# Kernel tuning notes

Hardware: AMD Instinct MI355X
Metric: run time of the kernel (lower is better)

Reference implementation:

```python
import jax, jax.numpy as jnp
import numpy as np

C1, C2, NHEAD = 256, 512, 8
HEAD_DIM = C1 // NHEAD
LN_EPS = 1e-5
L2_EPS = 1e-4
RMS_EPS = 1e-6
BN_EPS = 1e-5


def _linear(x, w, b):
    return x @ w.T + b


def _layernorm(x, w, b):
    mu = jnp.mean(x, axis=-1, keepdims=True)
    var = jnp.mean((x - mu) ** 2, axis=-1, keepdims=True)
    return (x - mu) / jnp.sqrt(var + LN_EPS) * w + b


def _rmsnorm(x, w):
    rms = jnp.sqrt(jnp.mean(x * x, axis=-1, keepdims=True) + RMS_EPS)
    return w * x / rms


def _l2norm(x):
    n = jnp.sqrt(jnp.sum(x * x, axis=-1, keepdims=True))
    return x / jnp.maximum(n, L2_EPS)


def _avg_pool(x, k):
    b, c, h, w = x.shape
    return x.reshape(b, c, h // k, k, w // k, k).mean(axis=(3, 5))


def _pos_embed_2d(w_, h_, dim, temperature=10000.0):
    # mirrors build_2d_sincos_position_embedding(w, h, embed_dim) called as (h, w, c)
    pos_dim = dim // 4
    omega = 1.0 / temperature ** (jnp.arange(pos_dim, dtype=jnp.float32) / pos_dim)
    gw, gh = jnp.meshgrid(jnp.arange(w_, dtype=jnp.float32),
                          jnp.arange(h_, dtype=jnp.float32), indexing='ij')
    ow = gw.reshape(-1, 1) * omega[None, :]
    oh = gh.reshape(-1, 1) * omega[None, :]
    return jnp.concatenate([jnp.sin(ow), jnp.cos(ow), jnp.sin(oh), jnp.cos(oh)], axis=1)  # [h*w, dim]


def setup_inputs() -> dict:
    key = jax.random.key(0)
    ks = jax.random.split(key, 32)
    p = lambda i, shape, s=0.02: jax.random.normal(ks[i], shape, dtype=jnp.float32) * s
    return {
        'a3': jax.random.normal(ks[0], (8, C1, 112, 112), dtype=jnp.float32),
        'a4': jax.random.normal(ks[1], (8, C2, 56, 56), dtype=jnp.float32),
        'conv_w': p(2, (C1, C2)), 'conv_b': p(3, (C1,)),
        'bn_w': 1.0 + p(4, (C1,)), 'bn_b': p(5, (C1,)),
        'q_w': p(6, (C1, C1)), 'q_b': p(7, (C1,)),
        'q_ln_w': 1.0 + p(8, (C1,)), 'q_ln_b': p(9, (C1,)),
        'k_w': p(10, (C1, C1)), 'k_b': p(11, (C1,)),
        'k_ln_w': 1.0 + p(12, (C1,)), 'k_ln_b': p(13, (C1,)),
        'v_w': p(14, (C1, C1)), 'v_b': p(15, (C1,)),
        'o_w': p(16, (C1, C1)), 'o_b': p(17, (C1,)),
        'rms_w': 1.0 + p(18, (HEAD_DIM,)),
        'l1_w': p(19, (4 * C1, C1)), 'l1_b': p(20, (4 * C1,)),
        'l2_w': p(21, (C1, 4 * C1)), 'l2_b': p(22, (C1,)),
        'n1_w': 1.0 + p(23, (C1,)), 'n1_b': p(24, (C1,)),
        'n2_w': 1.0 + p(25, (C1,)), 'n2_b': p(26, (C1,)),
        'idx': 10,
    }


def reference(a3, a4, conv_w, conv_b, bn_w, bn_b, q_w, q_b, q_ln_w, q_ln_b,
              k_w, k_b, k_ln_w, k_ln_b, v_w, v_b, o_w, o_b, rms_w,
              l1_w, l1_b, l2_w, l2_b, n1_w, n1_b, n2_w, n2_b, idx):
    # high_to_low_embed: 1x1 conv + BatchNorm2d (eval mode, running mean/var = 0/1)
    a4e = jnp.einsum('bchw,oc->bohw', a4, conv_w) + conv_b[None, :, None, None]
    a4e = a4e / np.float32(np.sqrt(1.0 + BN_EPS)) * bn_w[None, :, None, None] + bn_b[None, :, None, None]
    if idx == 10:
        a3_down = _avg_pool(a3, 2)
    else:
        a3_down = _avg_pool(a3, 4)
        a4e = _avg_pool(a4e, 2)
    b, c, h, w = a3_down.shape
    L = h * w
    residual = a3_down.reshape(b, c, L).transpose(0, 2, 1)   # [b, L, c]
    a3f = a3_down.reshape(b, c, L).transpose(2, 0, 1)        # [L, b, c]
    a4f = a4e.reshape(b, c, -1).transpose(2, 0, 1)           # [L, b, c]
    pos = _pos_embed_2d(h, w, c)[:, None, :]                 # [L, 1, c]
    a3f = a3f + pos
    a4f = a4f + pos
    Q = _layernorm(_linear(a3f, q_w, q_b), q_ln_w, q_ln_b)
    K = _layernorm(_linear(a4f, k_w, k_b), k_ln_w, k_ln_b)
    V = _linear(a4f, v_w, v_b)
    Q = _l2norm(Q)
    K = _l2norm(K)
    Q = Q.reshape(L, b * NHEAD, HEAD_DIM).transpose(1, 0, 2)  # [b*h, L, d]
    K = K.reshape(L, b * NHEAD, HEAD_DIM).transpose(1, 0, 2)
    V = V.reshape(L, b * NHEAD, HEAD_DIM).transpose(1, 0, 2)
    # cosFormer-style sin/cos positional reweighting (src_len == tgt_len here)
    wi = (jnp.arange(1, L + 1, dtype=jnp.float32) / L)[None, :, None]
    sw, cw = jnp.sin(wi), jnp.cos(wi)
    Q_ = jnp.concatenate([Q * cw, Q * sw], axis=-1)          # [b*h, L, 2d]
    K_ = jnp.concatenate([K * cw, K * sw], axis=-1)
    KV = jnp.einsum('nld,nlm->ndm', K_, V)                   # [b*h, 2d, d]
    attn = jnp.einsum('nld,ndm->nlm', Q_, KV)                # [b*h, L, d]
    attn = _rmsnorm(attn, rms_w)
    attn = attn.reshape(b, NHEAD, L, HEAD_DIM).transpose(2, 0, 1, 3).reshape(L, b, c)
    out = _linear(attn, o_w, o_b).transpose(1, 0, 2)         # [b, L, c]
    out = residual + _layernorm(out, n1_w, n1_b)
    residual2 = out
    ffn = _linear(jax.nn.gelu(_linear(out, l1_w, l1_b), approximate=False), l2_w, l2_b)
    out = residual2 + _layernorm(ffn, n2_w, n2_b)
    a3_sa = out.transpose(0, 2, 1).reshape(b, c, h, w)
    a3_sa = jax.image.resize(a3_sa, a3.shape, method='bilinear')  # align_corners=False
    a3_sa = a3_sa * a3
    b4, c4, h4, w4 = a4.shape
    a4_up = jax.image.resize(a4, (b4, c4, 2 * h4, 2 * w4), method='bilinear')
    return (a3_sa, a4_up)
```

## Files before the change

### kernel.cpp

```cpp
#include <hip/hip_runtime.h>
#include <math.h>

#define L_    3136
#define R_    25088
#define C_    256
#define MATF  6422528

typedef __attribute__((ext_vector_type(8))) short s16x8;
typedef __attribute__((ext_vector_type(4))) float f32x4;
typedef unsigned short us;

__device__ __forceinline__ us bfh(float v) {
    unsigned u = __float_as_uint(v);
    u = (u + 0x7FFFu + ((u >> 16) & 1u)) >> 16;
    return (us)u;
}
__device__ __forceinline__ float bf2f(us h) { return __uint_as_float((unsigned)h << 16); }
__device__ __forceinline__ void split2(float v, us& h, us& l) {
    h = bfh(v);
    l = bfh(v - bf2f(h));
}
__device__ __forceinline__ uint4 packu4(const us* s) {
    uint4 u;
    u.x = (unsigned)s[0] | ((unsigned)s[1] << 16);
    u.y = (unsigned)s[2] | ((unsigned)s[3] << 16);
    u.z = (unsigned)s[4] | ((unsigned)s[5] << 16);
    u.w = (unsigned)s[6] | ((unsigned)s[7] << 16);
    return u;
}
__device__ __forceinline__ uint2 packu2(const us* s) {
    uint2 u;
    u.x = (unsigned)s[0] | ((unsigned)s[1] << 16);
    u.y = (unsigned)s[2] | ((unsigned)s[3] << 16);
    return u;
}

__device__ __forceinline__ void gl16(const us* g, const us* l) {
    __builtin_amdgcn_global_load_lds(
        (const __attribute__((address_space(1))) unsigned int*)(unsigned long long)(const void*)g,
        (__attribute__((address_space(3))) unsigned int*)(unsigned int)(unsigned long long)(const void*)l,
        16, 0, 0);
}

__device__ __forceinline__ void wconv_body(const float* __restrict__ src,
        us* __restrict__ dh, us* __restrict__ dl, int idx, int kgs, int K)
{
    int m  = idx >> kgs;
    int gk = idx & ((1 << kgs) - 1);
    const float* sp = src + (size_t)m * K + gk * 8;
    float4 v0 = *(const float4*)sp;
    float4 v1 = *(const float4*)(sp + 4);
    float vv[8] = {v0.x, v0.y, v0.z, v0.w, v1.x, v1.y, v1.z, v1.w};
    us hh[8], ll[8];
    #pragma unroll
    for (int e = 0; e < 8; e++) split2(vv[e], hh[e], ll[e]);
    int p = gk ^ ((m >> 1) & 7);
    size_t off = (size_t)m * K + (size_t)p * 8;
    *(uint4*)(dh + off) = packu4(hh);
    *(uint4*)(dl + off) = packu4(ll);
}

__global__ __launch_bounds__(256)
void wconv1_k(const float* __restrict__ w, us* __restrict__ dh, us* __restrict__ dl)
{
    wconv_body(w, dh, dl, blockIdx.x * 256 + threadIdx.x, 6, 512);
}

__global__ __launch_bounds__(256)
void wconv6_k(const float* __restrict__ q, const float* __restrict__ k,
              const float* __restrict__ v, const float* __restrict__ o,
              const float* __restrict__ l1, const float* __restrict__ l2,
              us* __restrict__ wb)
{
    int bid = blockIdx.x;
    const float* src; us* dh; us* dl; int kgs, K;
    if (bid < 32)       { src = q;  dh = wb;           dl = wb + 65536;   kgs = 5; K = 256;  }
    else if (bid < 64)  { src = k;  dh = wb + 131072;  dl = wb + 196608;  kgs = 5; K = 256;  bid -= 32;  }
    else if (bid < 96)  { src = v;  dh = wb + 262144;  dl = wb + 327680;  kgs = 5; K = 256;  bid -= 64;  }
    else if (bid < 128) { src = o;  dh = wb + 393216;  dl = wb + 458752;  kgs = 5; K = 256;  bid -= 96;  }
    else if (bid < 256) { src = l1; dh = wb + 524288;  dl = wb + 786432;  kgs = 5; K = 256;  bid -= 128; }
    else                { src = l2; dh = wb + 1048576; dl = wb + 1310720; kgs = 7; K = 1024; bid -= 256; }
    wconv_body(src, dh, dl, bid * 256 + threadIdx.x, kgs, K);
}

__global__ __launch_bounds__(256)
void tconv_k(const float* __restrict__ src, us* __restrict__ dh, us* __restrict__ dl,
             int C, int Lb)
{
    __shared__ float tl[64][68];
    int l0 = blockIdx.x * 64, c0 = blockIdx.y * 64, b = blockIdx.z;
    int t = threadIdx.x;
    {
        int cl = t >> 2, qq = t & 3;
        const float* sp = src + ((size_t)b * C + c0 + cl) * Lb + l0 + qq * 16;
        #pragma unroll
        for (int i = 0; i < 4; i++) {
            float4 v = *(const float4*)(sp + i * 4);
            *(float4*)&tl[cl][qq * 16 + i * 4] = v;
        }
    }
    __syncthreads();
    int rl = t & 63, cq = t >> 6;
    size_t r = (size_t)b * Lb + l0 + rl;
    int s3 = ((l0 + rl) >> 1) & 7;
    size_t rowo = r * (size_t)C;
    #pragma unroll
    for (int half = 0; half < 2; half++) {
        us hh[8], ll[8];
        #pragma unroll
        for (int e = 0; e < 8; e++)
            split2(tl[cq * 16 + half * 8 + e][rl], hh[e], ll[e]);
        int gfull = (c0 >> 3) + cq * 2 + half;
        int p = gfull ^ s3;
        *(uint4*)(dh + rowo + (size_t)p * 8) = packu4(hh);
        *(uint4*)(dl + rowo + (size_t)p * 8) = packu4(ll);
    }
}

#define GBM 128
#define GBN 64
#define GBK 64
enum { GE_F32 = 0, GE_CONVT = 1, GE_GELUT = 2 };

template<int EPI>
__global__ __launch_bounds__(256)
void gemm_mf(const us* __restrict__ Wh, const us* __restrict__ Wl,
             const us* __restrict__ Xh, const us* __restrict__ Xl,
             float* __restrict__ Yf, us* __restrict__ Yth, us* __restrict__ Ytl,
             const float* __restrict__ bias, const float* __restrict__ bnw,
             const float* __restrict__ bnb, const float* __restrict__ pos,
             int K, int mts, int Mrow)
{
    __shared__ us Ah[GBM * GBK];
    __shared__ us Al[GBM * GBK];
    __shared__ us Bh[GBN * GBK];
    __shared__ us Bl[GBN * GBK];

    const int tid = threadIdx.x;
    int nwg = gridDim.x;
    int wg = (blockIdx.x & 7) * (nwg >> 3) + (blockIdx.x >> 3);
    int mt = wg & ((1 << mts) - 1);
    int rt = wg >> mts;
    const int m0 = mt * GBM;
    const int r0 = rt * GBN;

    const us* Ahg = Wh + (size_t)m0 * K;
    const us* Alg = Wl + (size_t)m0 * K;
    const us* Bhg = Xh + (size_t)r0 * K;
    const us* Blg = Xl + (size_t)r0 * K;

    const int lane = tid & 63;
    const int w    = tid >> 6;
    const int wm   = (w >> 1) * 64;
    const int wr   = (w & 1) * 32;
    const int l15  = lane & 15;
    const int lg   = lane >> 4;

    f32x4 acc[4][2];
    #pragma unroll
    for (int a = 0; a < 4; a++)
        #pragma unroll
        for (int b = 0; b < 2; b++)
            acc[a][b] = (f32x4){0.f, 0.f, 0.f, 0.f};

    for (int k0 = 0; k0 < K; k0 += GBK) {
        #pragma unroll
        for (int q = 0; q < 4; q++) {
            int g = q * 256 + tid;
            int row = g >> 3, sub = (g & 7) << 3;
            gl16(Ahg + (size_t)row * K + k0 + sub, Ah + g * 8);
            gl16(Alg + (size_t)row * K + k0 + sub, Al + g * 8);
        }
        #pragma unroll
        for (int q = 0; q < 2; q++) {
            int g = q * 256 + tid;
            int row = g >> 3, sub = (g & 7) << 3;
            gl16(Bhg + (size_t)row * K + k0 + sub, Bh + g * 8);
            gl16(Blg + (size_t)row * K + k0 + sub, Bl + g * 8);
        }
        __syncthreads();
        #pragma unroll
        for (int kk = 0; kk < 2; kk++) {
            s16x8 ah[4], al[4], bh[2], bl[2];
            #pragma unroll
            for (int a = 0; a < 4; a++) {
                int row = wm + a * 16 + l15;
                int p = ((kk << 2) | lg) ^ ((row >> 1) & 7);
                ah[a] = *(const s16x8*)(Ah + row * GBK + p * 8);
                al[a] = *(const s16x8*)(Al + row * GBK + p * 8);
            }
            #pragma unroll
            for (int b = 0; b < 2; b++) {
                int row = wr + b * 16 + l15;
                int p = ((kk << 2) | lg) ^ ((row >> 1) & 7);
                bh[b] = *(const s16x8*)(Bh + row * GBK + p * 8);
                bl[b] = *(const s16x8*)(Bl + row * GBK + p * 8);
            }
            #pragma unroll
            for (int a = 0; a < 4; a++)
                #pragma unroll
                for (int b = 0; b < 2; b++) {
                    acc[a][b] = __builtin_amdgcn_mfma_f32_16x16x32_bf16(ah[a], bh[b], acc[a][b], 0, 0, 0);
                    acc[a][b] = __builtin_amdgcn_mfma_f32_16x16x32_bf16(ah[a], bl[b], acc[a][b], 0, 0, 0);
                    acc[a][b] = __builtin_amdgcn_mfma_f32_16x16x32_bf16(al[a], bh[b], acc[a][b], 0, 0, 0);
                }
        }
        __syncthreads();
    }

    if (EPI == GE_F32) {
        #pragma unroll
        for (int a = 0; a < 4; a++) {
            int mb = m0 + wm + a * 16 + lg * 4;
            #pragma unroll
            for (int b = 0; b < 2; b++) {
                int rr = r0 + wr + b * 16 + l15;
                #pragma unroll
                for (int q = 0; q < 4; q++)
                    Yf[(size_t)(mb + q) * R_ + rr] = acc[a][b][q] + bias[mb + q];
            }
        }
    } else {
        #pragma unroll
        for (int b = 0; b < 2; b++) {
            int rr = r0 + wr + b * 16 + l15;
            int s3 = (rr >> 1) & 7;
            int l = rr % L_;
            size_t rowo = (size_t)rr * Mrow;
            #pragma unroll
            for (int a = 0; a < 4; a++) {
                int mb = m0 + wm + a * 16 + lg * 4;
                us hh[4], ll[4];
                #pragma unroll
                for (int q = 0; q < 4; q++) {
                    int m = mb + q;
                    float v = acc[a][b][q] + bias[m];
                    if (EPI == GE_CONVT) {
                        v = v * 0.9999950000374997f * bnw[m] + bnb[m];
                        v += pos[(size_t)m * L_ + l];
                    } else {
                        v = 0.5f * v * (1.f + erff(v * 0.7071067811865475f));
                    }
                    split2(v, hh[q], ll[q]);
                }
                int p = (mb >> 3) ^ s3;
                size_t off = rowo + (size_t)((p << 3) | (mb & 7));
                *(uint2*)(Yth + off) = packu2(hh);
                *(uint2*)(Ytl + off) = packu2(ll);
            }
        }
    }
}

__global__ __launch_bounds__(256)
void pos_k(float* __restrict__ pos)
{
    int c = blockIdx.x;
    int q = c >> 6, t = c & 63;
    float om = exp2f(-(float)t * (13.287712379549449f / 64.f));
    for (int l = threadIdx.x; l < L_; l += 256) {
        int y = l / 56, x = l - y * 56;
        float arg = (q < 2 ? (float)y : (float)x) * om;
        pos[(size_t)c * L_ + l] = (q & 1) ? cosf(arg) : sinf(arg);
    }
}

__global__ __launch_bounds__(256)
void pool_k(const float* __restrict__ a3, const float* __restrict__ pos,
            float* __restrict__ a3d, us* __restrict__ xh, us* __restrict__ xl)
{
    __shared__ us hi[256][34];
    __shared__ us lo[256][34];
    int blk = blockIdx.x;
    int b = blk / 98, l0 = (blk % 98) * 32;
    int t = threadIdx.x;
    {
        int lt = t & 31, cg = t >> 5;
        int l = l0 + lt;
        int y = l / 56, x = l - y * 56;
        const float* srow = a3 + ((size_t)b * 256) * 12544 + (2 * y) * 112 + 2 * x;
        float* drow = a3d + (size_t)b * L_ + l;
        const float* prow = pos + l;
        for (int cc = 0; cc < 32; cc++) {
            int c = cc * 8 + cg;
            const float* sp = srow + (size_t)c * 12544;
            float2 v0 = *(const float2*)sp;
            float2 v1 = *(const float2*)(sp + 112);
            float v = (v0.x + v0.y + v1.x + v1.y) * 0.25f;
            drow[(size_t)c * R_] = v;
            split2(v + prow[(size_t)c * L_], hi[c][lt], lo[c][lt]);
        }
    }
    __syncthreads();
    int j = t & 31, cq = t >> 5;
    int r = b * L_ + l0 + j;
    int s3 = ((l0 + j) >> 1) & 7;
    size_t rowo = (size_t)r * 256;
    #pragma unroll
    for (int gg = 0; gg < 4; gg++) {
        int cb = cq * 32 + gg * 8;
        us hh[8], ll[8];
        #pragma unroll
        for (int e = 0; e < 8; e++) { hh[e] = hi[cb + e][j]; ll[e] = lo[cb + e][j]; }
        int p = ((cq << 2) | gg) ^ s3;
        *(uint4*)(xh + rowo + (size_t)p * 8) = packu4(hh);
        *(uint4*)(xl + rowo + (size_t)p * 8) = packu4(ll);
    }
}

__global__ __launch_bounds__(256)
void ln_l2_k(float* __restrict__ X, const float* __restrict__ wt, const float* __restrict__ bt)
{
    __shared__ float red[4][64];
    __shared__ float red2[4][64];
    int tid = threadIdx.x;
    int rr = tid & 63, og = tid >> 6;
    size_t r = (size_t)blockIdx.x * 64 + rr;
    float s1 = 0.f, s2 = 0.f;
    for (int j = 0; j < 64; j++) {
        float v = X[(size_t)(og * 64 + j) * R_ + r];
        s1 += v; s2 = fmaf(v, v, s2);
    }
    red[og][rr] = s1; red2[og][rr] = s2;
    __syncthreads();
    float mu  = (red[0][rr] + red[1][rr] + red[2][rr] + red[3][rr]) * (1.f / 256.f);
    float var = (red2[0][rr] + red2[1][rr] + red2[2][rr] + red2[3][rr]) * (1.f / 256.f) - mu * mu;
    float rstd = rsqrtf(var + 1e-5f);
    __syncthreads();
    float t2 = 0.f;
    for (int j = 0; j < 64; j++) {
        int o = og * 64 + j;
        float v = X[(size_t)o * R_ + r];
        float y = (v - mu) * rstd * wt[o] + bt[o];
        t2 = fmaf(y, y, t2);
    }
    red[og][rr] = t2;
    __syncthreads();
    float nrm = sqrtf(red[0][rr] + red[1][rr] + red[2][rr] + red[3][rr]);
    float scale = 1.f / fmaxf(nrm, 1e-4f);
    for (int j = 0; j < 64; j++) {
        int o = og * 64 + j;
        size_t ix = (size_t)o * R_ + r;
        float v = X[ix];
        X[ix] = (v - mu) * rstd * wt[o] * scale + bt[o] * scale;
    }
}

template<int TOUT>
__global__ __launch_bounds__(256)
void ln_res_k(float* __restrict__ X, const float* __restrict__ res,
              const float* __restrict__ wt, const float* __restrict__ bt,
              us* __restrict__ th, us* __restrict__ tl_)
{
    __shared__ float red[4][64];
    __shared__ float red2[4][64];
    int tid = threadIdx.x;
    int rr = tid & 63, og = tid >> 6;
    size_t r = (size_t)blockIdx.x * 64 + rr;
    float s1 = 0.f, s2 = 0.f;
    for (int j = 0; j < 64; j++) {
        float v = X[(size_t)(og * 64 + j) * R_ + r];
        s1 += v; s2 = fmaf(v, v, s2);
    }
    red[og][rr] = s1; red2[og][rr] = s2;
    __syncthreads();
    float mu  = (red[0][rr] + red[1][rr] + red[2][rr] + red[3][rr]) * (1.f / 256.f);
    float var = (red2[0][rr] + red2[1][rr] + red2[2][rr] + red2[3][rr]) * (1.f / 256.f) - mu * mu;
    float rstd = rsqrtf(var + 1e-5f);
    float yv[64];
    #pragma unroll
    for (int j = 0; j < 64; j++) {
        int o = og * 64 + j;
        size_t ix = (size_t)o * R_ + r;
        float v = X[ix];
        float y = res[ix] + (v - mu) * rstd * wt[o] + bt[o];
        X[ix] = y;
        yv[j] = y;
    }
    if (TOUT) {
        int s3 = ((int)r >> 1) & 7;
        size_t rowo = r * 256;
        #pragma unroll
        for (int g = 0; g < 8; g++) {
            us hh[8], ll[8];
            #pragma unroll
            for (int e = 0; e < 8; e++) split2(yv[g * 8 + e], hh[e], ll[e]);
            int p = ((og << 3) | g) ^ s3;
            *(uint4*)(th  + rowo + (size_t)p * 8) = packu4(hh);
            *(uint4*)(tl_ + rowo + (size_t)p * 8) = packu4(ll);
        }
    }
}

__global__ __launch_bounds__(256)
void kv_part_k(const float* __restrict__ Kt, const float* __restrict__ Vt,
               float* __restrict__ kvp)
{
    __shared__ float kl[64][33];
    __shared__ float vl[64][33];
    __shared__ float cwl[64], swl[64];
    int slab = blockIdx.x;
    int n = blockIdx.y;
    int b = n >> 3, h = n & 7;
    int tid = threadIdx.x;
    int lane = tid & 63, grp = tid >> 6;
    int d = tid >> 2;
    int m0 = (tid & 3) * 8;
    float acc[8] = {0,0,0,0,0,0,0,0};
    size_t base = (size_t)(h * 32) * R_ + (size_t)b * L_;
    for (int ch = 0; ch < 7; ch++) {
        int l0 = slab * 448 + ch * 64;
        #pragma unroll
        for (int j = 0; j < 8; j++) {
            int dd = grp * 8 + j;
            kl[lane][dd] = Kt[base + (size_t)dd * R_ + l0 + lane];
            vl[lane][dd] = Vt[base + (size_t)dd * R_ + l0 + lane];
        }
        if (tid < 64) {
            float wi = (float)(l0 + tid + 1) * (1.f / 3136.f);
            cwl[tid] = cosf(wi); swl[tid] = sinf(wi);
        }
        __syncthreads();
        for (int l = 0; l < 64; l++) {
            float kvv = (d < 32 ? cwl[l] : swl[l]) * kl[l][d & 31];
            #pragma unroll
            for (int j = 0; j < 8; j++)
                acc[j] = fmaf(kvv, vl[l][m0 + j], acc[j]);
        }
        __syncthreads();
    }
    float* out = kvp + ((size_t)(n * 7 + slab)) * 2048 + d * 32 + m0;
    #pragma unroll
    for (int j = 0; j < 8; j++) out[j] = acc[j];
}

__global__ __launch_bounds__(256)
void kv_red_k(const float* __restrict__ kvp, float* __restrict__ kv)
{
    int idx = blockIdx.x * 256 + threadIdx.x;
    int n = idx >> 11, dm = idx & 2047;
    float s = 0.f;
    #pragma unroll
    for (int t = 0; t < 7; t++) s += kvp[((size_t)(n * 7 + t)) * 2048 + dm];
    kv[idx] = s;
}

__global__ __launch_bounds__(256)
void attn_k(const float* __restrict__ Q, const float* __restrict__ kv,
            const float* __restrict__ rmsw, us* __restrict__ Gh, us* __restrict__ Gl)
{
    __shared__ float kvl[2048];
    int h = blockIdx.y, b = blockIdx.z;
    int tid = threadIdx.x;
    int n = b * 8 + h;
    for (int i = tid; i < 2048; i += 256) kvl[i] = kv[(size_t)n * 2048 + i];
    __syncthreads();
    int l = blockIdx.x * 256 + tid;
    if (l >= L_) return;
    size_t r = (size_t)b * L_ + l;
    float qd[32];
    #pragma unroll
    for (int dd = 0; dd < 32; dd++) qd[dd] = Q[((size_t)(h * 32 + dd)) * R_ + r];
    float wi = (float)(l + 1) * (1.f / 3136.f);
    float cw = cosf(wi), sw = sinf(wi);
    float val[32]; float ss = 0.f;
    #pragma unroll
    for (int m = 0; m < 32; m++) {
        float s1 = 0.f, s2 = 0.f;
        #pragma unroll
        for (int dd = 0; dd < 32; dd++) {
            s1 = fmaf(qd[dd], kvl[dd * 32 + m], s1);
            s2 = fmaf(qd[dd], kvl[(dd + 32) * 32 + m], s2);
        }
        float v = cw * s1 + sw * s2;
        val[m] = v; ss = fmaf(v, v, ss);
    }
    float rinv = rsqrtf(ss * (1.f / 32.f) + 1e-6f);
    int s3 = (l >> 1) & 7;
    size_t rowo = r * 256;
    #pragma unroll
    for (int j = 0; j < 4; j++) {
        us hh[8], ll[8];
        #pragma unroll
        for (int e = 0; e < 8; e++) {
            float y = rmsw[j * 8 + e] * val[j * 8 + e] * rinv;
            split2(y, hh[e], ll[e]);
        }
        int p = ((h << 2) | j) ^ s3;
        *(uint4*)(Gh + rowo + (size_t)p * 8) = packu4(hh);
        *(uint4*)(Gl + rowo + (size_t)p * 8) = packu4(ll);
    }
}

__device__ __forceinline__ void bil_coord(int o, int lim, int& i0, int& i1, float& t)
{
    float f = o * 0.5f - 0.25f;
    float fl = floorf(f);
    t = f - fl;
    int i = (int)fl;
    i0 = i < 0 ? 0 : (i > lim ? lim : i);
    int ip = i + 1;
    i1 = ip < 0 ? 0 : (ip > lim ? lim : ip);
}

__global__ __launch_bounds__(256)
void up_a3_k(const float* __restrict__ out2, const float* __restrict__ a3,
             float* __restrict__ out)
{
    unsigned idx = blockIdx.x * 256u + threadIdx.x;
    int xo = idx % 112;
    unsigned t1 = idx / 112;
    int yo = t1 % 112;
    unsigned t2 = t1 / 112;
    int c = t2 & 255;
    int b = t2 >> 8;
    int x0, x1, y0, y1; float tx, ty;
    bil_coord(xo, 55, x0, x1, tx);
    bil_coord(yo, 55, y0, y1, ty);
    const float* src = out2 + (size_t)c * R_ + (size_t)b * L_;
    float v00 = src[y0 * 56 + x0], v01 = src[y0 * 56 + x1];
    float v10 = src[y1 * 56 + x0], v11 = src[y1 * 56 + x1];
    float v = (1.f - ty) * ((1.f - tx) * v00 + tx * v01) + ty * ((1.f - tx) * v10 + tx * v11);
    out[idx] = v * a3[idx];
}

__global__ __launch_bounds__(256)
void up_a4_k(const float* __restrict__ a4, float* __restrict__ out)
{
    unsigned idx = blockIdx.x * 256u + threadIdx.x;
    int xo = idx % 112;
    unsigned t1 = idx / 112;
    int yo = t1 % 112;
    unsigned t2 = t1 / 112;
    int c = t2 & 511;
    int b = t2 >> 9;
    int x0, x1, y0, y1; float tx, ty;
    bil_coord(xo, 55, x0, x1, tx);
    bil_coord(yo, 55, y0, y1, ty);
    const float* src = a4 + (size_t)(b * 512 + c) * 3136;
    float v00 = src[y0 * 56 + x0], v01 = src[y0 * 56 + x1];
    float v10 = src[y1 * 56 + x0], v11 = src[y1 * 56 + x1];
    out[idx] = (1.f - ty) * ((1.f - tx) * v00 + tx * v01) + ty * ((1.f - tx) * v10 + tx * v11);
}

extern "C" void kernel_launch(void* const* d_in, const int* in_sizes, int n_in,
                              void* d_out, int out_size, void* d_ws, size_t ws_size,
                              hipStream_t stream)
{
    const float* a3     = (const float*)d_in[0];
    const float* a4     = (const float*)d_in[1];
    const float* conv_w = (const float*)d_in[2];
    const float* conv_b = (const float*)d_in[3];
    const float* bn_w   = (const float*)d_in[4];
    const float* bn_b   = (const float*)d_in[5];
    const float* q_w    = (const float*)d_in[6];
    const float* q_b    = (const float*)d_in[7];
    const float* q_ln_w = (const float*)d_in[8];
    const float* q_ln_b = (const float*)d_in[9];
    const float* k_w    = (const float*)d_in[10];
    const float* k_b    = (const float*)d_in[11];
    const float* k_ln_w = (const float*)d_in[12];
    const float* k_ln_b = (const float*)d_in[13];
    const float* v_w    = (const float*)d_in[14];
    const float* v_b    = (const float*)d_in[15];
    const float* o_w    = (const float*)d_in[16];
    const float* o_b    = (const float*)d_in[17];
    const float* rms_w  = (const float*)d_in[18];
    const float* l1_w   = (const float*)d_in[19];
    const float* l1_b   = (const float*)d_in[20];
    const float* l2_w   = (const float*)d_in[21];
    const float* l2_b   = (const float*)d_in[22];
    const float* n1_w   = (const float*)d_in[23];
    const float* n1_b   = (const float*)d_in[24];
    const float* n2_w   = (const float*)d_in[25];
    const float* n2_b   = (const float*)d_in[26];
    (void)in_sizes; (void)n_in; (void)out_size;

    float* ws  = (float*)d_ws;
    float* pos = ws;
    float* P0  = ws + 802816;
    float* P1  = P0 + MATF;
    float* P2  = P1 + MATF;
    float* P3  = P2 + MATF;
    float* P4  = P3 + MATF;
    float* P5  = P4 + MATF;
    float* P6  = P5 + MATF;
    float* P7  = P6 + MATF;
    float* kvp = P7 + MATF;
    float* kvb = kvp + 917504;
    if (ws_size < (size_t)53231616 * 4) return;

    us* xqt_h = (us*)P4;  us* xqt_l = xqt_h + MATF;
    us* a4t_h = (us*)P5;  us* a4t_l = (us*)P6;
    us* Cxt_h = (us*)P1;  us* Cxt_l = Cxt_h + MATF;
    us* Gat_h = (us*)P4;  us* Gat_l = Gat_h + MATF;
    us* Hot_h = (us*)P1;  us* Hot_l = Hot_h + MATF;
    us* ffn_h = (us*)P4;  us* ffn_l = (us*)P6;
    float* Dq = P5;
    float* Ek = P6;
    float* Fv = P3;
    float* Ho = P2;
    us* wb   = (us*)pos;
    us* wc_h = (us*)kvp;  us* wc_l = wc_h + 131072;

    pos_k  <<<256, 256, 0, stream>>>(pos);
    wconv1_k<<<64, 256, 0, stream>>>(conv_w, wc_h, wc_l);
    tconv_k<<<dim3(49, 8, 8), 256, 0, stream>>>(a4, a4t_h, a4t_l, 512, 3136);
    pool_k <<<784, 256, 0, stream>>>(a3, pos, P0, xqt_h, xqt_l);
    gemm_mf<GE_CONVT><<<784, 256, 0, stream>>>(wc_h, wc_l, a4t_h, a4t_l,
        nullptr, Cxt_h, Cxt_l, conv_b, bn_w, bn_b, pos, 512, 1, 256);
    wconv6_k<<<384, 256, 0, stream>>>(q_w, k_w, v_w, o_w, l1_w, l2_w, wb);
    gemm_mf<GE_F32><<<784, 256, 0, stream>>>(wb, wb + 65536, xqt_h, xqt_l,
        Dq, nullptr, nullptr, q_b, nullptr, nullptr, nullptr, 256, 1, 256);
    ln_l2_k<<<392, 256, 0, stream>>>(Dq, q_ln_w, q_ln_b);
    gemm_mf<GE_F32><<<784, 256, 0, stream>>>(wb + 131072, wb + 196608, Cxt_h, Cxt_l,
        Ek, nullptr, nullptr, k_b, nullptr, nullptr, nullptr, 256, 1, 256);
    ln_l2_k<<<392, 256, 0, stream>>>(Ek, k_ln_w, k_ln_b);
    gemm_mf<GE_F32><<<784, 256, 0, stream>>>(wb + 262144, wb + 327680, Cxt_h, Cxt_l,
        Fv, nullptr, nullptr, v_b, nullptr, nullptr, nullptr, 256, 1, 256);
    kv_part_k<<<dim3(7, 64), 256, 0, stream>>>(Ek, Fv, kvp);
    kv_red_k<<<512, 256, 0, stream>>>(kvp, kvb);
    attn_k<<<dim3(13, 8, 8), 256, 0, stream>>>(Dq, kvb, rms_w, Gat_h, Gat_l);
    gemm_mf<GE_F32><<<784, 256, 0, stream>>>(wb + 393216, wb + 458752, Gat_h, Gat_l,
        Ho, nullptr, nullptr, o_b, nullptr, nullptr, nullptr, 256, 1, 256);
    ln_res_k<1><<<392, 256, 0, stream>>>(Ho, P0, n1_w, n1_b, Hot_h, Hot_l);
    gemm_mf<GE_GELUT><<<3136, 256, 0, stream>>>(wb + 524288, wb + 786432, Hot_h, Hot_l,
        nullptr, ffn_h, ffn_l, l1_b, nullptr, nullptr, nullptr, 256, 3, 1024);
    gemm_mf<GE_F32><<<784, 256, 0, stream>>>(wb + 1048576, wb + 1310720, ffn_h, ffn_l,
        Fv, nullptr, nullptr, l2_b, nullptr, nullptr, nullptr, 1024, 1, 256);
    ln_res_k<0><<<392, 256, 0, stream>>>(Fv, Ho, n2_w, n2_b, nullptr, nullptr);
    up_a3_k<<<100352, 256, 0, stream>>>(Fv, a3, (float*)d_out);
    up_a4_k<<<200704, 256, 0, stream>>>(a4, (float*)d_out + 25690112);
}
```

Before: 1.183 ms.

## Double-buffer GEMM LDS with BK=32, restructure upsample kernels, cache LN rows

The MFMA GEMM now uses a double-buffered LDS pipeline with a K-tile of 32, issuing the next stage's async global-to-LDS loads while the current tile is computed. The XOR swizzle is shrunk to 2 bits across every producer kernel to match the narrower tile. The two 2x bilinear upsample kernels now give each thread a 2x2 output quad with fixed 0.25/0.75 weights and vector float2 stores, so neighbouring source values are reused. ln_l2_k keeps the row in registers instead of re-reading X three times, at the cost of much higher register pressure.

```diff
diff --git a/kernel.cpp b/kernel.cpp
--- a/kernel.cpp
+++ b/kernel.cpp
@@ -42,6 +42,10 @@
         16, 0, 0);
 }
 
+__device__ __forceinline__ int swz2(int g, int s2) {
+    return (g & ~3) | ((g ^ s2) & 3);
+}
+
 __device__ __forceinline__ void wconv_body(const float* __restrict__ src,
         us* __restrict__ dh, us* __restrict__ dl, int idx, int kgs, int K)
 {
@@ -54,7 +58,7 @@
     us hh[8], ll[8];
     #pragma unroll
     for (int e = 0; e < 8; e++) split2(vv[e], hh[e], ll[e]);
-    int p = gk ^ ((m >> 1) & 7);
+    int p = swz2(gk, (m >> 1) & 3);
     size_t off = (size_t)m * K + (size_t)p * 8;
     *(uint4*)(dh + off) = packu4(hh);
     *(uint4*)(dl + off) = packu4(ll);
@@ -102,7 +106,7 @@
     __syncthreads();
     int rl = t & 63, cq = t >> 6;
     size_t r = (size_t)b * Lb + l0 + rl;
-    int s3 = ((l0 + rl) >> 1) & 7;
+    int s2 = ((l0 + rl) >> 1) & 3;
     size_t rowo = r * (size_t)C;
     #pragma unroll
     for (int half = 0; half < 2; half++) {
@@ -111,7 +115,7 @@
         for (int e = 0; e < 8; e++)
             split2(tl[cq * 16 + half * 8 + e][rl], hh[e], ll[e]);
         int gfull = (c0 >> 3) + cq * 2 + half;
-        int p = gfull ^ s3;
+        int p = swz2(gfull, s2);
         *(uint4*)(dh + rowo + (size_t)p * 8) = packu4(hh);
         *(uint4*)(dl + rowo + (size_t)p * 8) = packu4(ll);
     }
@@ -119,7 +123,7 @@
 
 #define GBM 128
 #define GBN 64
-#define GBK 64
+#define GBK 32
 enum { GE_F32 = 0, GE_CONVT = 1, GE_GELUT = 2 };
 
 template<int EPI>
@@ -131,10 +135,10 @@
              const float* __restrict__ bnb, const float* __restrict__ pos,
              int K, int mts, int Mrow)
 {
-    __shared__ us Ah[GBM * GBK];
-    __shared__ us Al[GBM * GBK];
-    __shared__ us Bh[GBN * GBK];
-    __shared__ us Bl[GBN * GBK];
+    __shared__ us Ah[2][GBM * GBK];
+    __shared__ us Al[2][GBM * GBK];
+    __shared__ us Bh[2][GBN * GBK];
+    __shared__ us Bl[2][GBN * GBK];
 
     const int tid = threadIdx.x;
     int nwg = gridDim.x;
@@ -155,6 +159,11 @@
     const int wr   = (w & 1) * 32;
     const int l15  = lane & 15;
     const int lg   = lane >> 4;
+    const int s2k  = (l15 >> 1) & 3;
+    const int koff = ((lg ^ s2k) & 3) << 3;
+
+    const int asub = (tid & 3) << 3;
+    const int brow = tid >> 2, bsub = (tid & 3) << 3;
 
     f32x4 acc[4][2];
     #pragma unroll
@@ -163,50 +172,55 @@
         for (int b = 0; b < 2; b++)
             acc[a][b] = (f32x4){0.f, 0.f, 0.f, 0.f};
 
-    for (int k0 = 0; k0 < K; k0 += GBK) {
-        #pragma unroll
-        for (int q = 0; q < 4; q++) {
-            int g = q * 256 + tid;
-            int row = g >> 3, sub = (g & 7) << 3;
-            gl16(Ahg + (size_t)row * K + k0 + sub, Ah + g * 8);
-            gl16(Alg + (size_t)row * K + k0 + sub, Al + g * 8);
-        }
-        #pragma unroll
-        for (int q = 0; q < 2; q++) {
-            int g = q * 256 + tid;
-            int row = g >> 3, sub = (g & 7) << 3;
-            gl16(Bhg + (size_t)row * K + k0 + sub, Bh + g * 8);
-            gl16(Blg + (size_t)row * K + k0 + sub, Bl + g * 8);
-        }
-        __syncthreads();
-        #pragma unroll
-        for (int kk = 0; kk < 2; kk++) {
-            s16x8 ah[4], al[4], bh[2], bl[2];
-            #pragma unroll
-            for (int a = 0; a < 4; a++) {
-                int row = wm + a * 16 + l15;
-                int p = ((kk << 2) | lg) ^ ((row >> 1) & 7);
-                ah[a] = *(const s16x8*)(Ah + row * GBK + p * 8);
-                al[a] = *(const s16x8*)(Al + row * GBK + p * 8);
-            }
+    const int nst = K >> 5;
+
+    #define STAGE(buf, k0)                                                        \
+    {                                                                             \
+        _Pragma("unroll")                                                         \
+        for (int q = 0; q < 2; q++) {                                             \
+            int g = q * 256 + tid;                                                \
+            int row = g >> 2;                                                     \
+            gl16(Ahg + (size_t)row * K + (k0) + asub, &Ah[buf][g * 8]);           \
+            gl16(Alg + (size_t)row * K + (k0) + asub, &Al[buf][g * 8]);           \
+        }                                                                         \
+        gl16(Bhg + (size_t)brow * K + (k0) + bsub, &Bh[buf][tid * 8]);            \
+        gl16(Blg + (size_t)brow * K + (k0) + bsub, &Bl[buf][tid * 8]);            \
+    }
+
+    STAGE(0, 0);
+    __syncthreads();
+    int cur = 0;
+    for (int s = 0; s < nst; s++) {
+        if (s + 1 < nst) STAGE(cur ^ 1, (s + 1) << 5);
+        const us* AHc = &Ah[cur][0];
+        const us* ALc = &Al[cur][0];
+        const us* BHc = &Bh[cur][0];
+        const us* BLc = &Bl[cur][0];
+        s16x8 va[4], wa[4], vb[2], ub[2];
+        #pragma unroll
+        for (int a = 0; a < 4; a++) {
+            int off = (wm + a * 16 + l15) * GBK + koff;
+            va[a] = *(const s16x8*)(AHc + off);
+            wa[a] = *(const s16x8*)(ALc + off);
+        }
+        #pragma unroll
+        for (int b = 0; b < 2; b++) {
+            int off = (wr + b * 16 + l15) * GBK + koff;
+            vb[b] = *(const s16x8*)(BHc + off);
+            ub[b] = *(const s16x8*)(BLc + off);
+        }
+        #pragma unroll
+        for (int a = 0; a < 4; a++)
             #pragma unroll
             for (int b = 0; b < 2; b++) {
-                int row = wr + b * 16 + l15;
-                int p = ((kk << 2) | lg) ^ ((row >> 1) & 7);
-                bh[b] = *(const s16x8*)(Bh + row * GBK + p * 8);
-                bl[b] = *(const s16x8*)(Bl + row * GBK + p * 8);
+                acc[a][b] = __builtin_amdgcn_mfma_f32_16x16x32_bf16(va[a], vb[b], acc[a][b], 0, 0, 0);
+                acc[a][b] = __builtin_amdgcn_mfma_f32_16x16x32_bf16(va[a], ub[b], acc[a][b], 0, 0, 0);
+                acc[a][b] = __builtin_amdgcn_mfma_f32_16x16x32_bf16(wa[a], vb[b], acc[a][b], 0, 0, 0);
             }
-            #pragma unroll
-            for (int a = 0; a < 4; a++)
-                #pragma unroll
-                for (int b = 0; b < 2; b++) {
-                    acc[a][b] = __builtin_amdgcn_mfma_f32_16x16x32_bf16(ah[a], bh[b], acc[a][b], 0, 0, 0);
-                    acc[a][b] = __builtin_amdgcn_mfma_f32_16x16x32_bf16(ah[a], bl[b], acc[a][b], 0, 0, 0);
-                    acc[a][b] = __builtin_amdgcn_mfma_f32_16x16x32_bf16(al[a], bh[b], acc[a][b], 0, 0, 0);
-                }
-        }
         __syncthreads();
-    }
+        cur ^= 1;
+    }
+    #undef STAGE
 
     if (EPI == GE_F32) {
         #pragma unroll
@@ -224,7 +238,7 @@
         #pragma unroll
         for (int b = 0; b < 2; b++) {
             int rr = r0 + wr + b * 16 + l15;
-            int s3 = (rr >> 1) & 7;
+            int s2r = (rr >> 1) & 3;
             int l = rr % L_;
             size_t rowo = (size_t)rr * Mrow;
             #pragma unroll
@@ -243,7 +257,7 @@
                     }
                     split2(v, hh[q], ll[q]);
                 }
-                int p = (mb >> 3) ^ s3;
+                int p = swz2(mb >> 3, s2r);
                 size_t off = rowo + (size_t)((p << 3) | (mb & 7));
                 *(uint2*)(Yth + off) = packu2(hh);
                 *(uint2*)(Ytl + off) = packu2(ll);
@@ -294,7 +308,7 @@
     __syncthreads();
     int j = t & 31, cq = t >> 5;
     int r = b * L_ + l0 + j;
-    int s3 = ((l0 + j) >> 1) & 7;
+    int s2 = ((l0 + j) >> 1) & 3;
     size_t rowo = (size_t)r * 256;
     #pragma unroll
     for (int gg = 0; gg < 4; gg++) {
@@ -302,7 +316,7 @@
         us hh[8], ll[8];
         #pragma unroll
         for (int e = 0; e < 8; e++) { hh[e] = hi[cb + e][j]; ll[e] = lo[cb + e][j]; }
-        int p = ((cq << 2) | gg) ^ s3;
+        int p = swz2((cq << 2) | gg, s2);
         *(uint4*)(xh + rowo + (size_t)p * 8) = packu4(hh);
         *(uint4*)(xl + rowo + (size_t)p * 8) = packu4(ll);
     }
@@ -310,6 +324,47 @@
 
 __global__ __launch_bounds__(256)
 void ln_l2_k(float* __restrict__ X, const float* __restrict__ wt, const float* __restrict__ bt)
+{
+    __shared__ float red[4][64];
+    __shared__ float red2[4][64];
+    int tid = threadIdx.x;
+    int rr = tid & 63, og = tid >> 6;
+    size_t r = (size_t)blockIdx.x * 64 + rr;
+    float vv[64];
+    float s1 = 0.f, s2 = 0.f;
+    for (int j = 0; j < 64; j++) {
+        float v = X[(size_t)(og * 64 + j) * R_ + r];
+        vv[j] = v;
+        s1 += v; s2 = fmaf(v, v, s2);
+    }
+    red[og][rr] = s1; red2[og][rr] = s2;
+    __syncthreads();
+    float mu  = (red[0][rr] + red[1][rr] + red[2][rr] + red[3][rr]) * (1.f / 256.f);
+    float var = (red2[0][rr] + red2[1][rr] + red2[2][rr] + red2[3][rr]) * (1.f / 256.f) - mu * mu;
+    float rstd = rsqrtf(var + 1e-5f);
+    __syncthreads();
+    float t2 = 0.f;
+    for (int j = 0; j < 64; j++) {
+        int o = og * 64 + j;
+        float y = (vv[j] - mu) * rstd * wt[o] + bt[o];
+        t2 = fmaf(y, y, t2);
+    }
+    red[og][rr] = t2;
+    __syncthreads();
+    float nrm = sqrtf(red[0][rr] + red[1][rr] + red[2][rr] + red[3][rr]);
+    float scale = 1.f / fmaxf(nrm, 1e-4f);
+    for (int j = 0; j < 64; j++) {
+        int o = og * 64 + j;
+        size_t ix = (size_t)o * R_ + r;
+        X[ix] = (vv[j] - mu) * rstd * wt[o] * scale + bt[o] * scale;
+    }
+}
+
+template<int TOUT>
+__global__ __launch_bounds__(256)
+void ln_res_k(float* __restrict__ X, const float* __restrict__ res,
+              const float* __restrict__ wt, const float* __restrict__ bt,
+              us* __restrict__ th, us* __restrict__ tl_)
 {
     __shared__ float red[4][64];
     __shared__ float red2[4][64];
@@ -326,47 +381,6 @@
     float mu  = (red[0][rr] + red[1][rr] + red[2][rr] + red[3][rr]) * (1.f / 256.f);
     float var = (red2[0][rr] + red2[1][rr] + red2[2][rr] + red2[3][rr]) * (1.f / 256.f) - mu * mu;
     float rstd = rsqrtf(var + 1e-5f);
-    __syncthreads();
-    float t2 = 0.f;
-    for (int j = 0; j < 64; j++) {
-        int o = og * 64 + j;
-        float v = X[(size_t)o * R_ + r];
-        float y = (v - mu) * rstd * wt[o] + bt[o];
-        t2 = fmaf(y, y, t2);
-    }
-    red[og][rr] = t2;
-    __syncthreads();
-    float nrm = sqrtf(red[0][rr] + red[1][rr] + red[2][rr] + red[3][rr]);
-    float scale = 1.f / fmaxf(nrm, 1e-4f);
-    for (int j = 0; j < 64; j++) {
-        int o = og * 64 + j;
-        size_t ix = (size_t)o * R_ + r;
-        float v = X[ix];
-        X[ix] = (v - mu) * rstd * wt[o] * scale + bt[o] * scale;
-    }
-}
-
-template<int TOUT>
-__global__ __launch_bounds__(256)
-void ln_res_k(float* __restrict__ X, const float* __restrict__ res,
-              const float* __restrict__ wt, const float* __restrict__ bt,
-              us* __restrict__ th, us* __restrict__ tl_)
-{
-    __shared__ float red[4][64];
-    __shared__ float red2[4][64];
-    int tid = threadIdx.x;
-    int rr = tid & 63, og = tid >> 6;
-    size_t r = (size_t)blockIdx.x * 64 + rr;
-    float s1 = 0.f, s2 = 0.f;
-    for (int j = 0; j < 64; j++) {
-        float v = X[(size_t)(og * 64 + j) * R_ + r];
-        s1 += v; s2 = fmaf(v, v, s2);
-    }
-    red[og][rr] = s1; red2[og][rr] = s2;
-    __syncthreads();
-    float mu  = (red[0][rr] + red[1][rr] + red[2][rr] + red[3][rr]) * (1.f / 256.f);
-    float var = (red2[0][rr] + red2[1][rr] + red2[2][rr] + red2[3][rr]) * (1.f / 256.f) - mu * mu;
-    float rstd = rsqrtf(var + 1e-5f);
     float yv[64];
     #pragma unroll
     for (int j = 0; j < 64; j++) {
@@ -378,14 +392,14 @@
         yv[j] = y;
     }
     if (TOUT) {
-        int s3 = ((int)r >> 1) & 7;
+        int s2r = ((int)r >> 1) & 3;
         size_t rowo = r * 256;
         #pragma unroll
         for (int g = 0; g < 8; g++) {
             us hh[8], ll[8];
             #pragma unroll
             for (int e = 0; e < 8; e++) split2(yv[g * 8 + e], hh[e], ll[e]);
-            int p = ((og << 3) | g) ^ s3;
+            int p = swz2((og << 3) | g, s2r);
             *(uint4*)(th  + rowo + (size_t)p * 8) = packu4(hh);
             *(uint4*)(tl_ + rowo + (size_t)p * 8) = packu4(ll);
         }
@@ -476,7 +490,7 @@
         val[m] = v; ss = fmaf(v, v, ss);
     }
     float rinv = rsqrtf(ss * (1.f / 32.f) + 1e-6f);
-    int s3 = (l >> 1) & 7;
+    int s2w = (l >> 1) & 3;
     size_t rowo = r * 256;
     #pragma unroll
     for (int j = 0; j < 4; j++) {
@@ -486,61 +500,78 @@
             float y = rmsw[j * 8 + e] * val[j * 8 + e] * rinv;
             split2(y, hh[e], ll[e]);
         }
-        int p = ((h << 2) | j) ^ s3;
+        int p = swz2((h << 2) | j, s2w);
         *(uint4*)(Gh + rowo + (size_t)p * 8) = packu4(hh);
         *(uint4*)(Gl + rowo + (size_t)p * 8) = packu4(ll);
     }
 }
 
-__device__ __forceinline__ void bil_coord(int o, int lim, int& i0, int& i1, float& t)
-{
-    float f = o * 0.5f - 0.25f;
-    float fl = floorf(f);
-    t = f - fl;
-    int i = (int)fl;
-    i0 = i < 0 ? 0 : (i > lim ? lim : i);
-    int ip = i + 1;
-    i1 = ip < 0 ? 0 : (ip > lim ? lim : ip);
-}
-
 __global__ __launch_bounds__(256)
 void up_a3_k(const float* __restrict__ out2, const float* __restrict__ a3,
              float* __restrict__ out)
 {
     unsigned idx = blockIdx.x * 256u + threadIdx.x;
-    int xo = idx % 112;
-    unsigned t1 = idx / 112;
-    int yo = t1 % 112;
-    unsigned t2 = t1 / 112;
+    int k = idx % 56;
+    unsigned t1 = idx / 56;
+    int j = t1 % 56;
+    unsigned t2 = t1 / 56;
     int c = t2 & 255;
     int b = t2 >> 8;
-    int x0, x1, y0, y1; float tx, ty;
-    bil_coord(xo, 55, x0, x1, tx);
-    bil_coord(yo, 55, y0, y1, ty);
+    int km = k > 0 ? k - 1 : 0, kp = k < 55 ? k + 1 : 55;
+    int jm = j > 0 ? j - 1 : 0, jp = j < 55 ? j + 1 : 55;
     const float* src = out2 + (size_t)c * R_ + (size_t)b * L_;
-    float v00 = src[y0 * 56 + x0], v01 = src[y0 * 56 + x1];
-    float v10 = src[y1 * 56 + x0], v11 = src[y1 * 56 + x1];
-    float v = (1.f - ty) * ((1.f - tx) * v00 + tx * v01) + ty * ((1.f - tx) * v10 + tx * v11);
-    out[idx] = v * a3[idx];
+    const float* r0 = src + jm * 56;
+    const float* r1 = src + j  * 56;
+    const float* r2 = src + jp * 56;
+    float h00 = fmaf(0.25f, r0[km], 0.75f * r0[k]);
+    float h01 = fmaf(0.25f, r0[kp], 0.75f * r0[k]);
+    float h10 = fmaf(0.25f, r1[km], 0.75f * r1[k]);
+    float h11 = fmaf(0.25f, r1[kp], 0.75f * r1[k]);
+    float h20 = fmaf(0.25f, r2[km], 0.75f * r2[k]);
+    float h21 = fmaf(0.25f, r2[kp], 0.75f * r2[k]);
+    float o00 = fmaf(0.25f, h00, 0.75f * h10);
+    float o01 = fmaf(0.25f, h01, 0.75f * h11);
+    float o10 = fmaf(0.25f, h20, 0.75f * h10);
+    float o11 = fmaf(0.25f, h21, 0.75f * h11);
+    size_t obase = (((size_t)(b * 256 + c) * 112) + 2 * j) * 112 + 2 * k;
+    const float* ap = a3 + obase;
+    float2 a0 = *(const float2*)ap;
+    float2 a1 = *(const float2*)(ap + 112);
+    float2 w0 = {o00 * a0.x, o01 * a0.y};
+    float2 w1 = {o10 * a1.x, o11 * a1.y};
+    *(float2*)(out + obase) = w0;
+    *(float2*)(out + obase + 112) = w1;
 }
 
 __global__ __launch_bounds__(256)
 void up_a4_k(const float* __restrict__ a4, float* __restrict__ out)
 {
     unsigned idx = blockIdx.x * 256u + threadIdx.x;
-    int xo = idx % 112;
-    unsigned t1 = idx / 112;
-    int yo = t1 % 112;
-    unsigned t2 = t1 / 112;
+    int k = idx % 56;
+    unsigned t1 = idx / 56;
+    int j = t1 % 56;
+    unsigned t2 = t1 / 56;
     int c = t2 & 511;
     int b = t2 >> 9;
-    int x0, x1, y0, y1; float tx, ty;
-    bil_coord(xo, 55, x0, x1, tx);
-    bil_coord(yo, 55, y0, y1, ty);
+    int km = k > 0 ? k - 1 : 0, kp = k < 55 ? k + 1 : 55;
+    int jm = j > 0 ? j - 1 : 0, jp = j < 55 ? j + 1 : 55;
     const float* src = a4 + (size_t)(b * 512 + c) * 3136;
-    float v00 = src[y0 * 56 + x0], v01 = src[y0 * 56 + x1];
-    float v10 = src[y1 * 56 + x0], v11 = src[y1 * 56 + x1];
-    out[idx] = (1.f - ty) * ((1.f - tx) * v00 + tx * v01) + ty * ((1.f - tx) * v10 + tx * v11);
+    const float* r0 = src + jm * 56;
+    const float* r1 = src + j  * 56;
+    const float* r2 = src + jp * 56;
+    float h00 = fmaf(0.25f, r0[km], 0.75f * r0[k]);
+    float h01 = fmaf(0.25f, r0[kp], 0.75f * r0[k]);
+    float h10 = fmaf(0.25f, r1[km], 0.75f * r1[k]);
+    float h11 = fmaf(0.25f, r1[kp], 0.75f * r1[k]);
+    float h20 = fmaf(0.25f, r2[km], 0.75f * r2[k]);
+    float h21 = fmaf(0.25f, r2[kp], 0.75f * r2[k]);
+    float o00 = fmaf(0.25f, h00, 0.75f * h10);
+    float o01 = fmaf(0.25f, h01, 0.75f * h11);
+    float o10 = fmaf(0.25f, h20, 0.75f * h10);
+    float o11 = fmaf(0.25f, h21, 0.75f * h11);
+    size_t obase = (((size_t)(b * 512 + c) * 112) + 2 * j) * 112 + 2 * k;
+    *(float2*)(out + obase) = (float2){o00, o01};
+    *(float2*)(out + obase + 112) = (float2){o10, o11};
 }
 
 extern "C" void kernel_launch(void* const* d_in, const int* in_sizes, int n_in,
@@ -629,6 +660,6 @@
     gemm_mf<GE_F32><<<784, 256, 0, stream>>>(wb + 1048576, wb + 1310720, ffn_h, ffn_l,
         Fv, nullptr, nullptr, l2_b, nullptr, nullptr, nullptr, 1024, 1, 256);
     ln_res_k<0><<<392, 256, 0, stream>>>(Fv, Ho, n2_w, n2_b, nullptr, nullptr);
-    up_a3_k<<<100352, 256, 0, stream>>>(Fv, a3, (float*)d_out);
-    up_a4_k<<<200704, 256, 0, stream>>>(a4, (float*)d_out + 25690112);
-}
+    up_a3_k<<<25088, 256, 0, stream>>>(Fv, a3, (float*)d_out);
+    up_a4_k<<<50176, 256, 0, stream>>>(a4, (float*)d_out + 25690112);
+}
```

After: 1.102 ms. -6.9%, faster.
